# Kernel tuning notes

Measured on AMD Instinct MI355X. Metric: run time of the kernel, lower is better.

The kernel has to match this reference:

```python
import jax, jax.numpy as jnp
import numpy as np

B, T, D = 2, 2048, 1024
H, G, K = 16, 4, 64          # num_heads, num_kv_heads, head_dim
R = H // G                   # GQA repeat factor
F = 4096                     # mlp_dim
EPS = 1e-6


def rms_norm(x, scale, eps=EPS):
    var = jnp.mean(x.astype(jnp.float32) ** 2, axis=-1, keepdims=True)
    normed = x * jax.lax.rsqrt(var + eps)
    return (scale * normed).astype(x.dtype)


def apply_rope(x_BTHK, sin_BTK, cos_BTK):
    half = x_BTHK.shape[-1] // 2
    x1, x2 = x_BTHK[..., :half], x_BTHK[..., half:]
    s = sin_BTK[:, :, None, :]
    c = cos_BTK[:, :, None, :]
    return jnp.concatenate([x1 * c - x2 * s, x2 * c + x1 * s], axis=-1).astype(x_BTHK.dtype)


def setup_inputs() -> dict:
    key = jax.random.key(0)
    ks = jax.random.split(key, 12)
    hidden_BTD = jax.random.normal(ks[0], (B, T, D), jnp.float32)
    # rope tables: realistic sin/cos of position*inv_freq
    inv_freq = 1.0 / (10000.0 ** (jnp.arange(K // 2, dtype=jnp.float32) / (K // 2)))
    ang = jnp.arange(T, dtype=jnp.float32)[:, None] * inv_freq[None, :]  # [T, K/2]
    sin_BTK = jnp.broadcast_to(jnp.sin(ang)[None], (B, T, K // 2))
    cos_BTK = jnp.broadcast_to(jnp.cos(ang)[None], (B, T, K // 2))
    mask = jnp.broadcast_to(jnp.tril(jnp.ones((T, T), bool))[None], (B, T, T))
    sc = 1.0 / np.sqrt(D)
    scf = 1.0 / np.sqrt(F)
    return {
        "hidden_BTD": hidden_BTD, "sin_BTK": sin_BTK, "cos_BTK": cos_BTK, "mask": mask,
        "ln1_scale": jnp.ones((D,), jnp.float32),
        "ln2_scale": jnp.ones((D,), jnp.float32),
        "qn_scale": jnp.ones((K,), jnp.float32),
        "kn_scale": jnp.ones((K,), jnp.float32),
        "q_w": jax.random.normal(ks[1], (D, H * K), jnp.float32) * sc,
        "k_w": jax.random.normal(ks[2], (D, G * K), jnp.float32) * sc,
        "v_w": jax.random.normal(ks[3], (D, G * K), jnp.float32) * sc,
        "o_w": jax.random.normal(ks[4], (H * K, D), jnp.float32) * sc,
        "gate_w": jax.random.normal(ks[5], (D, F), jnp.float32) * sc,
        "up_w": jax.random.normal(ks[6], (D, F), jnp.float32) * sc,
        "down_w": jax.random.normal(ks[7], (F, D), jnp.float32) * scf,
    }


def reference(hidden_BTD, sin_BTK, cos_BTK, mask, ln1_scale, ln2_scale,
              qn_scale, kn_scale, q_w, k_w, v_w, o_w, gate_w, up_w, down_w):
    x = rms_norm(hidden_BTD, ln1_scale)
    q = rms_norm((x @ q_w).reshape(B, T, H, K), qn_scale)
    k = rms_norm((x @ k_w).reshape(B, T, G, K), kn_scale)
    v = (x @ v_w).reshape(B, T, G, K)
    q = apply_rope(q, sin_BTK, cos_BTK)
    k = apply_rope(k, sin_BTK, cos_BTK)
    q_BTGRK = q.reshape(B, T, G, R, K)
    scale = K ** (-0.5)
    logits = jnp.einsum('BTGRK,BSGK->BTSGR', q_BTGRK, k) * scale
    neg = float(jnp.finfo(logits.dtype).min)
    logits = jnp.where(mask[:, :, :, None, None], logits, neg)
    weights = jax.nn.softmax(logits.astype(jnp.float32), axis=2).astype(logits.dtype)
    attn = jnp.einsum('BTSGR,BSGK->BTGRK', weights, v).reshape(B, T, H * K)
    hidden_BTD = hidden_BTD + attn @ o_w
    y = rms_norm(hidden_BTD, ln2_scale)
    ff = (jax.nn.silu(y @ gate_w) * (y @ up_w)) @ down_w
    return hidden_BTD + ff
```

## Files before the change

kernel.cpp:

```cpp
#include <hip/hip_runtime.h>
#include <hip/hip_bf16.h>

#define EPSF 1e-6f
constexpr int Bsz  = 2;
constexpr int Tseq = 2048;
constexpr int Dmod = 1024;
constexpr int Hh   = 16;
constexpr int Gg   = 4;
constexpr int Ff   = 4096;
constexpr int Mrows = Bsz * Tseq;

typedef __attribute__((ext_vector_type(8))) short bf16x8;
typedef __attribute__((ext_vector_type(4))) float f32x4;
typedef unsigned short u16;

__device__ inline u16 f2bf(float x) {
    union { float f; unsigned u; } v; v.f = x;
    unsigned r = v.u + 0x7fff + ((v.u >> 16) & 1);
    return (u16)(r >> 16);
}
__device__ inline float bf2f(u16 h) {
    union { unsigned u; float f; } v; v.u = ((unsigned)h) << 16; return v.f;
}

__device__ __forceinline__ void async_copy16(const u16* g, u16* l) {
    __builtin_amdgcn_global_load_lds(
        (const __attribute__((address_space(1))) void*)g,
        (__attribute__((address_space(3))) void*)l, 16, 0, 0);
}


__global__ __launch_bounds__(256) void wprep_all_kernel(
    const float* __restrict__ q_w, const float* __restrict__ k_w,
    const float* __restrict__ v_w, const float* __restrict__ o_w,
    const float* __restrict__ gate_w, const float* __restrict__ up_w,
    const float* __restrict__ down_w,
    const float* __restrict__ hidden, const float* __restrict__ ln1,
    u16* __restrict__ QKVT, u16* __restrict__ OTh, u16* __restrict__ OTl,
    u16* __restrict__ GTh, u16* __restrict__ UTh, u16* __restrict__ DTh,
    u16* __restrict__ Xh)
{
    const int bx = blockIdx.x;

    if (bx >= 14848) {
        const int row = bx - 14848;
        const int tid = threadIdx.x;
        const float4 v = reinterpret_cast<const float4*>(hidden + (size_t)row * Dmod)[tid];
        float ss = v.x * v.x + v.y * v.y + v.z * v.z + v.w * v.w;
        #pragma unroll
        for (int off = 32; off; off >>= 1) ss += __shfl_xor(ss, off, 64);
        __shared__ float part[4];
        if ((tid & 63) == 0) part[tid >> 6] = ss;
        __syncthreads();
        const float tot = part[0] + part[1] + part[2] + part[3];
        const float rstd = rsqrtf(tot * (1.0f / Dmod) + EPSF);
        const float4 sc = reinterpret_cast<const float4*>(ln1)[tid];
        ushort4 h;
        h.x = f2bf(v.x * rstd * sc.x); h.y = f2bf(v.y * rstd * sc.y);
        h.z = f2bf(v.z * rstd * sc.z); h.w = f2bf(v.w * rstd * sc.w);
        *reinterpret_cast<ushort4*>(&Xh[(size_t)row * Dmod + tid * 4]) = h;
        return;
    }

    const float* W; u16* Th; u16* Tl = nullptr;
    int N, Kd, ntile, ktile, drow;
    if (bx < 1024) {
        W = q_w; N = 1024; Kd = 1024; ntile = bx & 31; ktile = bx >> 5;
        Th = QKVT; drow = ntile * 32;
    } else if (bx < 1280) {
        const int i = bx - 1024;
        W = k_w; N = 256; Kd = 1024; ntile = i & 7; ktile = i >> 3;
        Th = QKVT; drow = 1024 + ntile * 32;
    } else if (bx < 1536) {
        const int i = bx - 1280;
        W = v_w; N = 256; Kd = 1024; ntile = i & 7; ktile = i >> 3;
        Th = QKVT; drow = 1280 + ntile * 32;
    } else if (bx < 2560) {
        const int i = bx - 1536;
        W = o_w; N = 1024; Kd = 1024; ntile = i & 31; ktile = i >> 5;
        Th = OTh; Tl = OTl; drow = ntile * 32;
    } else if (bx < 6656) {
        const int i = bx - 2560;
        W = gate_w; N = 4096; Kd = 1024; ntile = i & 127; ktile = i >> 7;
        Th = GTh; drow = ntile * 32;
    } else if (bx < 10752) {
        const int i = bx - 6656;
        W = up_w; N = 4096; Kd = 1024; ntile = i & 127; ktile = i >> 7;
        Th = UTh; drow = ntile * 32;
    } else {
        const int i = bx - 10752;
        W = down_w; N = 1024; Kd = 4096; ntile = i & 31; ktile = i >> 5;
        Th = DTh; drow = ntile * 32;
    }
    const int n0 = ntile * 32, k0 = ktile * 32;

    __shared__ float tile[32][33];
    const int r = threadIdx.x >> 3, c4 = (threadIdx.x & 7) * 4;
    const float4 v = *reinterpret_cast<const float4*>(&W[(size_t)(k0 + r) * N + n0 + c4]);
    tile[r][c4 + 0] = v.x; tile[r][c4 + 1] = v.y;
    tile[r][c4 + 2] = v.z; tile[r][c4 + 3] = v.w;
    __syncthreads();
    const int nl = threadIdx.x >> 3, kq = (threadIdx.x & 7) * 4;
    float x0 = tile[kq + 0][nl], x1 = tile[kq + 1][nl];
    float x2 = tile[kq + 2][nl], x3 = tile[kq + 3][nl];
    ushort4 h;
    h.x = f2bf(x0); h.y = f2bf(x1); h.z = f2bf(x2); h.w = f2bf(x3);
    *reinterpret_cast<ushort4*>(&Th[(size_t)(drow + nl) * Kd + k0 + kq]) = h;
    if (Tl) {
        ushort4 l;
        l.x = f2bf(x0 - bf2f(h.x)); l.y = f2bf(x1 - bf2f(h.y));
        l.z = f2bf(x2 - bf2f(h.z)); l.w = f2bf(x3 - bf2f(h.w));
        *reinterpret_cast<ushort4*>(&Tl[(size_t)(drow + nl) * Kd + k0 + kq]) = l;
    }
}

template <int LO>
__global__ __launch_bounds__(256) void rmsnorm_split_kernel(
    const float* __restrict__ x, const float* __restrict__ scale,
    u16* __restrict__ oh, u16* __restrict__ ol)
{
    const int row = blockIdx.x;
    const int tid = threadIdx.x;
    const float4 v = reinterpret_cast<const float4*>(x + (size_t)row * Dmod)[tid];
    float ss = v.x * v.x + v.y * v.y + v.z * v.z + v.w * v.w;
    #pragma unroll
    for (int off = 32; off; off >>= 1) ss += __shfl_xor(ss, off, 64);
    __shared__ float part[4];
    if ((tid & 63) == 0) part[tid >> 6] = ss;
    __syncthreads();
    const float tot = part[0] + part[1] + part[2] + part[3];
    const float rstd = rsqrtf(tot * (1.0f / Dmod) + EPSF);
    const float4 sc = reinterpret_cast<const float4*>(scale)[tid];
    float o0 = v.x * rstd * sc.x, o1 = v.y * rstd * sc.y;
    float o2 = v.z * rstd * sc.z, o3 = v.w * rstd * sc.w;
    ushort4 h;
    h.x = f2bf(o0); h.y = f2bf(o1); h.z = f2bf(o2); h.w = f2bf(o3);
    *reinterpret_cast<ushort4*>(&oh[(size_t)row * Dmod + tid * 4]) = h;
    if (LO) {
        ushort4 l;
        l.x = f2bf(o0 - bf2f(h.x)); l.y = f2bf(o1 - bf2f(h.y));
        l.z = f2bf(o2 - bf2f(h.z)); l.w = f2bf(o3 - bf2f(h.w));
        *reinterpret_cast<ushort4*>(&ol[(size_t)row * Dmod + tid * 4]) = l;
    }
}

template <int NKT, int BN, int ASPLIT, int BSPLIT, int RES>
__global__ __launch_bounds__(256, 2) void mfma_gemm_pipe(
    const u16* __restrict__ Ah, const u16* __restrict__ Al,
    const u16* __restrict__ Bh, const u16* __restrict__ Bl,
    const float* __restrict__ res, float* __restrict__ C,
    int M, int N)
{
    constexpr int Kd = NKT * 32;
    constexpr int NT = (BN / 2) / 16;
    constexpr int NI = 2 + 2 * ASPLIT + (BN / 64) + (BN / 64) * BSPLIT;
    static_assert((NKT - 2) % 3 == 0, "main loop unroll-3");

    __shared__ u16 AsH[3][128 * 32];
    __shared__ u16 BsH[3][BN * 32];
    __shared__ u16 AsL[ASPLIT ? 3 : 1][128 * 32];
    __shared__ u16 BsL[BSPLIT ? 3 : 1][BN * 32];

    const int tid = threadIdx.x;
    const int lane = tid & 63, wave = tid >> 6;
    const int wm = (wave >> 1) * 64, wn = (wave & 1) * (BN / 2);
    const int m0 = blockIdx.y * 128, n0 = blockIdx.x * BN;
    const int fm = lane & 15, quad = lane >> 4;
    const int fsw = (fm >> 1) & 3;
    const int fcol = (quad ^ fsw) * 8;

    f32x4 acc[4][NT];
    #pragma unroll
    for (int i = 0; i < 4; ++i)
        #pragma unroll
        for (int j = 0; j < NT; ++j) acc[i][j] = (f32x4){0.f, 0.f, 0.f, 0.f};

    const int srow = tid >> 2;
    const int schk = tid & 3;
    const int sw   = schk ^ ((srow >> 1) & 3);
    const u16* aS0 = &Ah[(size_t)(m0 + srow) * Kd + sw * 8];
    const u16* aS1 = &Ah[(size_t)(m0 + srow + 64) * Kd + sw * 8];
    const u16* bS0 = &Bh[(size_t)(n0 + srow) * Kd + sw * 8];
    const u16* bS1 = (BN == 128) ? &Bh[(size_t)(n0 + srow + 64) * Kd + sw * 8] : nullptr;
    const u16* alS0 = ASPLIT ? &Al[(size_t)(m0 + srow) * Kd + sw * 8] : nullptr;
    const u16* alS1 = ASPLIT ? &Al[(size_t)(m0 + srow + 64) * Kd + sw * 8] : nullptr;
    const u16* blS0 = BSPLIT ? &Bl[(size_t)(n0 + srow) * Kd + sw * 8] : nullptr;
    const u16* blS1 = (BSPLIT && BN == 128) ? &Bl[(size_t)(n0 + srow + 64) * Kd + sw * 8] : nullptr;
    const int dst0 = srow * 32 + schk * 8;
    const int dst1 = dst0 + 64 * 32;

#define PSTAGE(T, BUF) do {                                                  \
        async_copy16(aS0 + (T) * 32, &AsH[BUF][dst0]);                       \
        async_copy16(aS1 + (T) * 32, &AsH[BUF][dst1]);                       \
        if (ASPLIT) {                                                        \
            async_copy16(alS0 + (T) * 32, &AsL[BUF][dst0]);                  \
            async_copy16(alS1 + (T) * 32, &AsL[BUF][dst1]);                  \
        }                                                                    \
        async_copy16(bS0 + (T) * 32, &BsH[BUF][dst0]);                       \
        if (BN == 128) async_copy16(bS1 + (T) * 32, &BsH[BUF][dst1]);        \
        if (BSPLIT) {                                                        \
            async_copy16(blS0 + (T) * 32, &BsL[BUF][dst0]);                  \
            if (BN == 128) async_copy16(blS1 + (T) * 32, &BsL[BUF][dst1]);   \
        }                                                                    \
    } while (0)

#define PGATE(GATE) do {                                                     \
        if ((GATE) == 1) {                                                   \
            if constexpr (NI == 3)                                           \
                asm volatile("s_waitcnt vmcnt(3)" ::: "memory");             \
            else if constexpr (NI == 4)                                      \
                asm volatile("s_waitcnt vmcnt(4)" ::: "memory");             \
            else if constexpr (NI == 6)                                      \
                asm volatile("s_waitcnt vmcnt(6)" ::: "memory");             \
            else                                                             \
                asm volatile("s_waitcnt vmcnt(8)" ::: "memory");             \
        } else if ((GATE) == 0) {                                            \
            asm volatile("s_waitcnt vmcnt(0)" ::: "memory");                 \
        }                                                                    \
    } while (0)

#define PSTEP(BC, BN_, T, PF, GATE) do {                                     \
    bf16x8 ah[4], bh[NT], al[4], bl[NT];                                     \
    _Pragma("unroll")                                                        \
    for (int t = 0; t < 4; ++t) {                                            \
        const int ra = (wm + t * 16 + fm) * 32 + fcol;                       \
        ah[t] = *reinterpret_cast<const bf16x8*>(&AsH[BC][ra]);              \
        if (ASPLIT) al[t] = *reinterpret_cast<const bf16x8*>(&AsL[BC][ra]);  \
    }                                                                        \
    _Pragma("unroll")                                                        \
    for (int t = 0; t < NT; ++t) {                                           \
        const int rb = (wn + t * 16 + fm) * 32 + fcol;                       \
        bh[t] = *reinterpret_cast<const bf16x8*>(&BsH[BC][rb]);              \
        if (BSPLIT) bl[t] = *reinterpret_cast<const bf16x8*>(&BsL[BC][rb]);  \
    }                                                                        \
    if (PF) PSTAGE((T) + 2, BN_);                                            \
    __builtin_amdgcn_s_setprio(1);                                           \
    _Pragma("unroll")                                                        \
    for (int mt = 0; mt < 4; ++mt)                                           \
        _Pragma("unroll")                                                    \
        for (int nt = 0; nt < NT; ++nt) {                                    \
            acc[mt][nt] = __builtin_amdgcn_mfma_f32_16x16x32_bf16(           \
                ah[mt], bh[nt], acc[mt][nt], 0, 0, 0);                       \
            if (BSPLIT)                                                      \
                acc[mt][nt] = __builtin_amdgcn_mfma_f32_16x16x32_bf16(       \
                    ah[mt], bl[nt], acc[mt][nt], 0, 0, 0);                   \
            if (ASPLIT)                                                      \
                acc[mt][nt] = __builtin_amdgcn_mfma_f32_16x16x32_bf16(       \
                    al[mt], bh[nt], acc[mt][nt], 0, 0, 0);                   \
        }                                                                    \
    __builtin_amdgcn_s_setprio(0);                                           \
    PGATE(GATE);                                                             \
    __builtin_amdgcn_s_barrier();                                            \
} while (0)

    PSTAGE(0, 0);
    PSTAGE(1, 1);
    PGATE(1);
    __builtin_amdgcn_s_barrier();

    #pragma unroll 1
    for (int t3 = 0; t3 < NKT - 2; t3 += 3) {
        PSTEP(0, 2, t3 + 0, true, 1);
        PSTEP(1, 0, t3 + 1, true, 1);
        PSTEP(2, 1, t3 + 2, true, 1);
    }
    PSTEP(0, 2, NKT - 2, false, 0);
    PSTEP(1, 0, NKT - 1, false, -1);

#undef PSTEP
#undef PGATE
#undef PSTAGE

    const int cr = (lane >> 4) * 4, cn = lane & 15;
    #pragma unroll
    for (int mt = 0; mt < 4; ++mt)
        #pragma unroll
        for (int nt = 0; nt < NT; ++nt)
            #pragma unroll
            for (int r = 0; r < 4; ++r) {
                const int gm = m0 + wm + mt * 16 + cr + r;
                const int gn = n0 + wn + nt * 16 + cn;
                float v = acc[mt][nt][r];
                if (RES) v += res[(size_t)gm * N + gn];
                C[(size_t)gm * N + gn] = v;
            }
}

__global__ __launch_bounds__(256, 2) void qkv_fused_kernel(
    const u16* __restrict__ Ah, const u16* __restrict__ Bh,
    const float* __restrict__ qn, const float* __restrict__ kn,
    const float* __restrict__ sinp, const float* __restrict__ cosp,
    u16* __restrict__ Qbh, u16* __restrict__ Qbl,
    u16* __restrict__ Kbh, u16* __restrict__ Kbl,
    u16* __restrict__ Vth, u16* __restrict__ Vtl)
{
    constexpr int Kd = 1024;
    constexpr int NKT = 32;
    __shared__ u16 As[3][128 * 32];
    __shared__ u16 Bs[3][128 * 32];

    const int tid = threadIdx.x;
    const int lane = tid & 63, wave = tid >> 6;
    const int wm = (wave >> 1) * 64, wn = (wave & 1) * 64;
    const int m0 = blockIdx.y * 128, n0 = blockIdx.x * 128;
    const int fm = lane & 15, quad = lane >> 4;
    const int fsw = (fm >> 1) & 3;
    const int fcol = ((quad ^ fsw) * 8);

    f32x4 acc[4][4];
    #pragma unroll
    for (int i = 0; i < 4; ++i)
        #pragma unroll
        for (int j = 0; j < 4; ++j) acc[i][j] = (f32x4){0.f, 0.f, 0.f, 0.f};

    const int srow = tid >> 2;
    const int schk = tid & 3;
    const int sw   = schk ^ ((srow >> 1) & 3);
    const u16* aS0 = &Ah[(size_t)(m0 + srow) * Kd + sw * 8];
    const u16* aS1 = &Ah[(size_t)(m0 + srow + 64) * Kd + sw * 8];
    const u16* bS0 = &Bh[(size_t)(n0 + srow) * Kd + sw * 8];
    const u16* bS1 = &Bh[(size_t)(n0 + srow + 64) * Kd + sw * 8];
    const int dst0 = srow * 32 + schk * 8;
    const int dst1 = dst0 + 64 * 32;

#define QSTAGE(T, BUF) do {                                                  \
        async_copy16(aS0 + (T) * 32, &As[BUF][dst0]);                        \
        async_copy16(aS1 + (T) * 32, &As[BUF][dst1]);                        \
        async_copy16(bS0 + (T) * 32, &Bs[BUF][dst0]);                        \
        async_copy16(bS1 + (T) * 32, &Bs[BUF][dst1]);                        \
    } while (0)

#define QSTEP(BC, BN, T, PF, GATE) do {                                      \
    bf16x8 ah[4], bh[4];                                                     \
    _Pragma("unroll")                                                        \
    for (int t = 0; t < 4; ++t) {                                            \
        ah[t] = *reinterpret_cast<const bf16x8*>(                            \
            &As[BC][(wm + t * 16 + fm) * 32 + fcol]);                        \
        bh[t] = *reinterpret_cast<const bf16x8*>(                            \
            &Bs[BC][(wn + t * 16 + fm) * 32 + fcol]);                        \
    }                                                                        \
    if (PF) QSTAGE((T) + 2, BN);                                             \
    __builtin_amdgcn_s_setprio(1);                                           \
    _Pragma("unroll")                                                        \
    for (int mt = 0; mt < 4; ++mt)                                           \
        _Pragma("unroll")                                                    \
        for (int nt = 0; nt < 4; ++nt)                                       \
            acc[mt][nt] = __builtin_amdgcn_mfma_f32_16x16x32_bf16(           \
                ah[mt], bh[nt], acc[mt][nt], 0, 0, 0);                       \
    __builtin_amdgcn_s_setprio(0);                                           \
    if ((GATE) == 1) {                                                       \
        asm volatile("s_waitcnt vmcnt(4)" ::: "memory");                     \
    } else if ((GATE) == 0) {                                                \
        asm volatile("s_waitcnt vmcnt(0)" ::: "memory");                     \
    }                                                                        \
    __builtin_amdgcn_s_barrier();                                            \
} while (0)

    QSTAGE(0, 0);
    QSTAGE(1, 1);
    asm volatile("s_waitcnt vmcnt(4)" ::: "memory");
    __builtin_amdgcn_s_barrier();

    #pragma unroll 1
    for (int t3 = 0; t3 < NKT - 2; t3 += 3) {
        QSTEP(0, 2, t3 + 0, true, 1);
        QSTEP(1, 0, t3 + 1, true, 1);
        QSTEP(2, 1, t3 + 2, true, 1);
    }
    QSTEP(0, 2, NKT - 2, false, 0);
    QSTEP(1, 0, NKT - 1, false, -1);

#undef QSTEP
#undef QSTAGE

    const int gn0 = n0 + wn;
    const int l15 = lane & 15;

    if (gn0 < 1280) {
        const bool isQ = (gn0 < 1024);
        const float* nsc = isQ ? qn : kn;
        const float osc = isQ ? 0.125f : 1.0f;
        u16* __restrict__ oh = isQ ? Qbh : Kbh;
        u16* __restrict__ ol = isQ ? Qbl : Kbl;
        const int rowstride = isQ ? 1024 : 256;
        const int colbase = isQ ? gn0 : gn0 - 1024;
        float sc[4];
        #pragma unroll
        for (int nt = 0; nt < 4; ++nt) sc[nt] = nsc[nt * 16 + l15];

        #pragma unroll
        for (int mt = 0; mt < 4; ++mt)
            #pragma unroll
            for (int r = 0; r < 4; ++r) {
                const int bt = m0 + wm + mt * 16 + quad * 4 + r;
                float v[4];
                #pragma unroll
                for (int nt = 0; nt < 4; ++nt) v[nt] = acc[mt][nt][r];
                float ss = v[0] * v[0] + v[1] * v[1] + v[2] * v[2] + v[3] * v[3];
                #pragma unroll
                for (int off = 1; off < 16; off <<= 1)
                    ss += __shfl_xor(ss, off, 16);
                const float rstd = rsqrtf(ss * (1.0f / 64.0f) + EPSF);
                float nv[4];
                #pragma unroll
                for (int nt = 0; nt < 4; ++nt) nv[nt] = v[nt] * rstd * sc[nt];
                const float s0 = sinp[bt * 32 + l15];
                const float c0 = cosp[bt * 32 + l15];
                const float s1 = sinp[bt * 32 + 16 + l15];
                const float c1 = cosp[bt * 32 + 16 + l15];
                float o[4];
                o[0] = (nv[0] * c0 - nv[2] * s0) * osc;
                o[1] = (nv[1] * c1 - nv[3] * s1) * osc;
                o[2] = (nv[2] * c0 + nv[0] * s0) * osc;
                o[3] = (nv[3] * c1 + nv[1] * s1) * osc;
                #pragma unroll
                for (int nt = 0; nt < 4; ++nt) {
                    const size_t off = (size_t)bt * rowstride + colbase + nt * 16 + l15;
                    const u16 hi = f2bf(o[nt]);
                    oh[off] = hi;
                    ol[off] = f2bf(o[nt] - bf2f(hi));
                }
            }
    } else {
        const int g = (gn0 - 1280) >> 6;
        const int b = (m0 + wm) >> 11;
        const int tb = ((m0 + wm) & 2047) + quad * 4;
        #pragma unroll
        for (int mt = 0; mt < 4; ++mt)
            #pragma unroll
            for (int nt = 0; nt < 4; ++nt) {
                const float v0 = acc[mt][nt][0], v1 = acc[mt][nt][1];
                const float v2 = acc[mt][nt][2], v3 = acc[mt][nt][3];
                ushort4 hv, lv;
                hv.x = f2bf(v0); hv.y = f2bf(v1); hv.z = f2bf(v2); hv.w = f2bf(v3);
                lv.x = f2bf(v0 - bf2f(hv.x)); lv.y = f2bf(v1 - bf2f(hv.y));
                lv.z = f2bf(v2 - bf2f(hv.z)); lv.w = f2bf(v3 - bf2f(hv.w));
                const size_t off =
                    ((size_t)((b * 4 + g) * 64 + nt * 16 + l15)) * Tseq + tb + mt * 16;
                *reinterpret_cast<ushort4*>(&Vth[off]) = hv;
                *reinterpret_cast<ushort4*>(&Vtl[off]) = lv;
            }
    }
}

#define GU_MFMA4(MBASE, AF)                                                      \
    _Pragma("unroll")                                                            \
    for (int mf = 0; mf < 4; ++mf) {                                             \
        accg[(MBASE) + mf][0] = __builtin_amdgcn_mfma_f32_16x16x32_bf16(         \
            AF[mf], bgf[0], accg[(MBASE) + mf][0], 0, 0, 0);                     \
        accu[(MBASE) + mf][0] = __builtin_amdgcn_mfma_f32_16x16x32_bf16(         \
            AF[mf], buf2[0], accu[(MBASE) + mf][0], 0, 0, 0);                    \
        accg[(MBASE) + mf][1] = __builtin_amdgcn_mfma_f32_16x16x32_bf16(         \
            AF[mf], bgf[1], accg[(MBASE) + mf][1], 0, 0, 0);                     \
        accu[(MBASE) + mf][1] = __builtin_amdgcn_mfma_f32_16x16x32_bf16(         \
            AF[mf], buf2[1], accu[(MBASE) + mf][1], 0, 0, 0);                    \
    }

__global__ __launch_bounds__(512, 2) void gateup8_kernel(
    const u16* __restrict__ Yh, const u16* __restrict__ Yl,
    const u16* __restrict__ Gw, const u16* __restrict__ Uw,
    u16* __restrict__ FF)
{
    constexpr int NK = 32;
    __shared__ u16 AsH[3][256 * 32];
    __shared__ u16 AsL[3][256 * 32];
    __shared__ u16 Gs[3][128 * 32];
    __shared__ u16 Us[3][128 * 32];

    const int tid  = threadIdx.x;
    const int lane = tid & 63;
    const int wave = tid >> 6;
    const int wave_m = wave >> 2;
    const int wave_n = wave & 3;

    const int wg  = blockIdx.x;
    const int xcd = wg & 7;
    const int idx = wg >> 3;
    const int ntile = xcd * 4 + (idx & 3);
    const int mtile = idx >> 2;
    const int m0 = mtile * 256, n0 = ntile * 128;

    const int fm = lane & 15, quad = lane >> 4;
    const int fsw = (fm >> 1) & 3;
    const int fcol = (quad ^ fsw) * 8;

    f32x4 accg[8][2], accu[8][2];
    #pragma unroll
    for (int i = 0; i < 8; ++i)
        #pragma unroll
        for (int j = 0; j < 2; ++j) {
            accg[i][j] = (f32x4){0.f, 0.f, 0.f, 0.f};
            accu[i][j] = (f32x4){0.f, 0.f, 0.f, 0.f};
        }

    const int srow = tid >> 2;
    const int schk = tid & 3;
    const int sw   = schk ^ ((srow >> 1) & 3);
    const u16* aSrc0 = &Yh[(size_t)(m0 + srow) * 1024 + sw * 8];
    const u16* aSrc1 = &Yh[(size_t)(m0 + srow + 128) * 1024 + sw * 8];
    const u16* lSrc0 = &Yl[(size_t)(m0 + srow) * 1024 + sw * 8];
    const u16* lSrc1 = &Yl[(size_t)(m0 + srow + 128) * 1024 + sw * 8];
    const u16* gSrc  = &Gw[(size_t)(n0 + srow) * 1024 + sw * 8];
    const u16* uSrc  = &Uw[(size_t)(n0 + srow) * 1024 + sw * 8];
    const int aDst0 = srow * 32 + schk * 8;
    const int aDst1 = aDst0 + 128 * 32;

#define STAGE_AH(T, BUF) do {                                  \
        async_copy16(aSrc0 + (T) * 32, &AsH[BUF][aDst0]);      \
        async_copy16(aSrc1 + (T) * 32, &AsH[BUF][aDst1]); } while (0)
#define STAGE_AL(T, BUF) do {                                  \
        async_copy16(lSrc0 + (T) * 32, &AsL[BUF][aDst0]);      \
        async_copy16(lSrc1 + (T) * 32, &AsL[BUF][aDst1]); } while (0)
#define STAGE_B(T, BUF) do {                                   \
        async_copy16(gSrc + (T) * 32, &Gs[BUF][aDst0]);        \
        async_copy16(uSrc + (T) * 32, &Us[BUF][aDst0]); } while (0)

    int raOff[8], rbOff[2];
    #pragma unroll
    for (int mf = 0; mf < 8; ++mf)
        raOff[mf] = (wave_m * 128 + mf * 16 + fm) * 32 + fcol;
    #pragma unroll
    for (int nf = 0; nf < 2; ++nf)
        rbOff[nf] = (wave_n * 32 + nf * 16 + fm) * 32 + fcol;

    STAGE_AH(0, 0); STAGE_AL(0, 0); STAGE_B(0, 0);
    STAGE_AH(1, 1); STAGE_AL(1, 1); STAGE_B(1, 1);
    asm volatile("s_waitcnt vmcnt(6)" ::: "memory");
    __builtin_amdgcn_s_barrier();

#define GU_STEP(BC, BN_, T, PF, GATE) do {                                   \
    bf16x8 bgf[2], buf2[2];                                                  \
    _Pragma("unroll")                                                        \
    for (int nf = 0; nf < 2; ++nf) {                                         \
        bgf[nf]  = *reinterpret_cast<const bf16x8*>(&Gs[BC][rbOff[nf]]);     \
        buf2[nf] = *reinterpret_cast<const bf16x8*>(&Us[BC][rbOff[nf]]);     \
    }                                                                        \
    {                                                                        \
        bf16x8 af[4];                                                        \
        _Pragma("unroll")                                                    \
        for (int mf = 0; mf < 4; ++mf)                                       \
            af[mf] = *reinterpret_cast<const bf16x8*>(&AsH[BC][raOff[mf]]);  \
        if (PF) STAGE_AH((T) + 2, BN_);                                      \
        __builtin_amdgcn_s_setprio(1);                                       \
        GU_MFMA4(0, af);                                                     \
        __builtin_amdgcn_s_setprio(0);                                       \
    }                                                                        \
    {                                                                        \
        bf16x8 af[4];                                                        \
        _Pragma("unroll")                                                    \
        for (int mf = 0; mf < 4; ++mf)                                       \
            af[mf] = *reinterpret_cast<const bf16x8*>(&AsH[BC][raOff[mf + 4]]); \
        if (PF) STAGE_AL((T) + 2, BN_);                                      \
        __builtin_amdgcn_s_setprio(1);                                       \
        GU_MFMA4(4, af);                                                     \
        __builtin_amdgcn_s_setprio(0);                                       \
    }                                                                        \
    {                                                                        \
        bf16x8 af[4];                                                        \
        _Pragma("unroll")                                                    \
        for (int mf = 0; mf < 4; ++mf)                                       \
            af[mf] = *reinterpret_cast<const bf16x8*>(&AsL[BC][raOff[mf]]);  \
        if (PF) STAGE_B((T) + 2, BN_);                                       \
        __builtin_amdgcn_s_setprio(1);                                       \
        GU_MFMA4(0, af);                                                     \
        __builtin_amdgcn_s_setprio(0);                                       \
    }                                                                        \
    {                                                                        \
        bf16x8 af[4];                                                        \
        _Pragma("unroll")                                                    \
        for (int mf = 0; mf < 4; ++mf)                                       \
            af[mf] = *reinterpret_cast<const bf16x8*>(&AsL[BC][raOff[mf + 4]]); \
        __builtin_amdgcn_s_setprio(1);                                       \
        GU_MFMA4(4, af);                                                     \
        __builtin_amdgcn_s_setprio(0);                                       \
    }                                                                        \
    if ((GATE) == 1) {                                                       \
        asm volatile("s_waitcnt vmcnt(6)" ::: "memory");                     \
    } else if ((GATE) == 0) {                                                \
        asm volatile("s_waitcnt vmcnt(0)" ::: "memory");                     \
    }                                                                        \
    __builtin_amdgcn_s_barrier();                                            \
} while (0)

    #pragma unroll 1
    for (int t3 = 0; t3 < NK - 2; t3 += 3) {
        GU_STEP(0, 2, t3 + 0, true, 1);
        GU_STEP(1, 0, t3 + 1, true, 1);
        GU_STEP(2, 1, t3 + 2, true, 1);
    }
    GU_STEP(0, 2, 30, false, 0);
    GU_STEP(1, 0, 31, false, -1);

#undef GU_STEP
#undef STAGE_AH
#undef STAGE_AL
#undef STAGE_B

    const int cr = quad * 4;
    #pragma unroll
    for (int mf = 0; mf < 8; ++mf)
        #pragma unroll
        for (int nf = 0; nf < 2; ++nf)
            #pragma unroll
            for (int r = 0; r < 4; ++r) {
                const int gm = m0 + wave_m * 128 + mf * 16 + cr + r;
                const int gn = n0 + wave_n * 32 + nf * 16 + fm;
                const float g = accg[mf][nf][r];
                const float ff = (g / (1.0f + __expf(-g))) * accu[mf][nf][r];
                FF[(size_t)gm * Ff + gn] = f2bf(ff);
            }
}

__global__ __launch_bounds__(512) void attn_mfma_kernel(
    const u16* __restrict__ Qh, const u16* __restrict__ Ql,
    const u16* __restrict__ Kh, const u16* __restrict__ Kl,
    const u16* __restrict__ Vth, const u16* __restrict__ Vtl,
    u16* __restrict__ AOh, u16* __restrict__ AOl)
{
    __shared__ u16 KsH[64 * 72];
    __shared__ u16 KsL[64 * 72];
    __shared__ u16 VsH[64 * 72];
    __shared__ u16 VsL[64 * 72];
    __shared__ u16 Ps[8][16 * 72];

    const int tid = threadIdx.x;
    const int wave = tid >> 6, lane = tid & 63;
    const int l15 = lane & 15, quad = lane >> 4;

    const int bg = blockIdx.x & 7;
    const int b = bg >> 2, g = bg & 3;
    const int pair = 63 - (blockIdx.x >> 3);
    const int win = pair * 2 + (wave >> 2);
    const int t0 = win * 16;
    const int h = g * 4 + (wave & 3);

    bf16x8 qh[2], ql[2];
    {
        const size_t qrow = (size_t)(b * Tseq + t0 + l15) * 1024 + h * 64;
        #pragma unroll
        for (int ks = 0; ks < 2; ++ks) {
            qh[ks] = *reinterpret_cast<const bf16x8*>(&Qh[qrow + ks * 32 + quad * 8]);
            ql[ks] = *reinterpret_cast<const bf16x8*>(&Ql[qrow + ks * 32 + quad * 8]);
        }
    }

    const int srow = tid >> 3;
    const int scol = (tid & 7) * 8;
    const size_t kgb = (size_t)(b * Tseq) * 256 + g * 64 + scol;
    const size_t vgb = (size_t)(bg * 64 + srow) * Tseq + scol;

    const int nit = (pair * 32 + 16) / 64 + 1;

    uint4 ck0, cl0, cv0, cw0;
    {
        const size_t ka = kgb + (size_t)srow * 256;
        ck0 = *reinterpret_cast<const uint4*>(&Kh[ka]);
        cl0 = *reinterpret_cast<const uint4*>(&Kl[ka]);
        cv0 = *reinterpret_cast<const uint4*>(&Vth[vgb]);
        cw0 = *reinterpret_cast<const uint4*>(&Vtl[vgb]);
    }

    f32x4 oacc[4];
    #pragma unroll
    for (int nt = 0; nt < 4; ++nt) oacc[nt] = (f32x4){0.f, 0.f, 0.f, 0.f};
    float m_r[4], l_r[4];
    #pragma unroll
    for (int r = 0; r < 4; ++r) { m_r[r] = -1e30f; l_r[r] = 0.0f; }

    u16* psw = &Ps[wave][0];
    const int lb = srow * 72 + scol;

    for (int it = 0; it < nit; ++it) {
        const int s0 = it * 64;
        const bool diag = (it == nit - 1);

        __syncthreads();
        *reinterpret_cast<uint4*>(&KsH[lb]) = ck0;
        *reinterpret_cast<uint4*>(&KsL[lb]) = cl0;
        *reinterpret_cast<uint4*>(&VsH[lb]) = cv0;
        *reinterpret_cast<uint4*>(&VsL[lb]) = cw0;
        if (it + 1 < nit) {
            const size_t ka = kgb + (size_t)(s0 + 64 + srow) * 256;
            ck0 = *reinterpret_cast<const uint4*>(&Kh[ka]);
            cl0 = *reinterpret_cast<const uint4*>(&Kl[ka]);
            const size_t va = vgb + s0 + 64;
            cv0 = *reinterpret_cast<const uint4*>(&Vth[va]);
            cw0 = *reinterpret_cast<const uint4*>(&Vtl[va]);
        }
        __syncthreads();

        f32x4 sacc[4];
        #pragma unroll
        for (int nt = 0; nt < 4; ++nt) sacc[nt] = (f32x4){0.f, 0.f, 0.f, 0.f};

        #pragma unroll
        for (int ks = 0; ks < 2; ++ks) {
            bf16x8 kfh[4], kfl[4];
            #pragma unroll
            for (int nt = 0; nt < 4; ++nt) {
                const int a = (nt * 16 + l15) * 72 + ks * 32 + quad * 8;
                kfh[nt] = *reinterpret_cast<const bf16x8*>(&KsH[a]);
                kfl[nt] = *reinterpret_cast<const bf16x8*>(&KsL[a]);
            }
            #pragma unroll
            for (int nt = 0; nt < 4; ++nt) {
                sacc[nt] = __builtin_amdgcn_mfma_f32_16x16x32_bf16(qh[ks], kfh[nt], sacc[nt], 0, 0, 0);
                sacc[nt] = __builtin_amdgcn_mfma_f32_16x16x32_bf16(ql[ks], kfh[nt], sacc[nt], 0, 0, 0);
                sacc[nt] = __builtin_amdgcn_mfma_f32_16x16x32_bf16(qh[ks], kfl[nt], sacc[nt], 0, 0, 0);
            }
        }

        if (diag) {
            #pragma unroll
            for (int nt = 0; nt < 4; ++nt) {
                const int sg = s0 + nt * 16 + l15;
                #pragma unroll
                for (int r = 0; r < 4; ++r)
                    if (sg > t0 + quad * 4 + r) sacc[nt][r] = -1e30f;
            }
        }

        #pragma unroll
        for (int r = 0; r < 4; ++r) {
            float mx = fmaxf(fmaxf(sacc[0][r], sacc[1][r]),
                             fmaxf(sacc[2][r], sacc[3][r]));
            #pragma unroll
            for (int off = 1; off < 16; off <<= 1)
                mx = fmaxf(mx, __shfl_xor(mx, off, 16));
            const float mnew = fmaxf(m_r[r], mx);
            const float alpha = __expf(m_r[r] - mnew);
            m_r[r] = mnew;

            float rs = 0.0f;
            #pragma unroll
            for (int nt = 0; nt < 4; ++nt) {
                const float p = __expf(sacc[nt][r] - mnew);
                sacc[nt][r] = p;
                rs += p;
            }
            #pragma unroll
            for (int off = 1; off < 16; off <<= 1)
                rs += __shfl_xor(rs, off, 16);
            l_r[r] = l_r[r] * alpha + rs;
            #pragma unroll
            for (int nt = 0; nt < 4; ++nt) oacc[nt][r] *= alpha;
            #pragma unroll
            for (int nt = 0; nt < 4; ++nt)
                psw[(quad * 4 + r) * 72 + nt * 16 + l15] = f2bf(sacc[nt][r]);
        }

        #pragma unroll
        for (int ks = 0; ks < 2; ++ks) {
            const bf16x8 pa = *reinterpret_cast<const bf16x8*>(
                &psw[l15 * 72 + ks * 32 + quad * 8]);
            bf16x8 vfh[4], vfl[4];
            #pragma unroll
            for (int nt = 0; nt < 4; ++nt) {
                const int a = (nt * 16 + l15) * 72 + ks * 32 + quad * 8;
                vfh[nt] = *reinterpret_cast<const bf16x8*>(&VsH[a]);
                vfl[nt] = *reinterpret_cast<const bf16x8*>(&VsL[a]);
            }
            #pragma unroll
            for (int nt = 0; nt < 4; ++nt) {
                oacc[nt] = __builtin_amdgcn_mfma_f32_16x16x32_bf16(pa, vfh[nt], oacc[nt], 0, 0, 0);
                oacc[nt] = __builtin_amdgcn_mfma_f32_16x16x32_bf16(pa, vfl[nt], oacc[nt], 0, 0, 0);
            }
        }
    }

    #pragma unroll
    for (int r = 0; r < 4; ++r) {
        const float inv = 1.0f / l_r[r];
        const size_t orow = (size_t)(b * Tseq + t0 + quad * 4 + r) * 1024 + h * 64;
        #pragma unroll
        for (int nt = 0; nt < 4; ++nt) {
            const float o = oacc[nt][r] * inv;
            const u16 hi = f2bf(o);
            AOh[orow + nt * 16 + l15] = hi;
            AOl[orow + nt * 16 + l15] = f2bf(o - bf2f(hi));
        }
    }
}

extern "C" void kernel_launch(void* const* d_in, const int* in_sizes, int n_in,
                              void* d_out, int out_size, void* d_ws,
                              size_t ws_size, hipStream_t stream)
{
    const float* hidden = (const float*)d_in[0];
    const float* sinp   = (const float*)d_in[1];
    const float* cosp   = (const float*)d_in[2];
    const float* ln1    = (const float*)d_in[4];
    const float* ln2    = (const float*)d_in[5];
    const float* qn     = (const float*)d_in[6];
    const float* kn     = (const float*)d_in[7];
    const float* q_w    = (const float*)d_in[8];
    const float* k_w    = (const float*)d_in[9];
    const float* v_w    = (const float*)d_in[10];
    const float* o_w    = (const float*)d_in[11];
    const float* gate_w = (const float*)d_in[12];
    const float* up_w   = (const float*)d_in[13];
    const float* down_w = (const float*)d_in[14];
    float* out = (float*)d_out;

    char* base = (char*)d_ws;
    u16*   OTh  = (u16*)(base);
    u16*   OTl  = (u16*)(base + 2097152);
    u16*   GTh  = (u16*)(base + 4194304);
    u16*   UTh  = (u16*)(base + 12582912);
    u16*   DTh  = (u16*)(base + 20971520);
    u16*   QKVT = (u16*)(base + 29360128);
    u16*   Xh   = (u16*)(base + 32505856);
    u16*   Qbh  = (u16*)(base + 40894464);
    u16*   Qbl  = (u16*)(base + 49283072);
    u16*   Kbh  = (u16*)(base + 57671680);
    u16*   Kbl  = (u16*)(base + 59768832);
    u16*   Vth  = (u16*)(base + 61865984);
    u16*   Vtl  = (u16*)(base + 63963136);
    u16*   AOh  = (u16*)(base + 66060288);
    u16*   AOl  = (u16*)(base + 74448896);
    u16*   FFh  = (u16*)(base + 82837504);

    float* H2 = (float*)Qbh;
    u16*   Yh = Kbh;
    u16*   Yl = AOh;

    wprep_all_kernel<<<14848 + Mrows, 256, 0, stream>>>(
        q_w, k_w, v_w, o_w, gate_w, up_w, down_w, hidden, ln1,
        QKVT, OTh, OTl, GTh, UTh, DTh, Xh);

    qkv_fused_kernel<<<dim3(12, 32), 256, 0, stream>>>(
        Xh, QKVT, qn, kn, sinp, cosp, Qbh, Qbl, Kbh, Kbl, Vth, Vtl);

    attn_mfma_kernel<<<Bsz * Gg * (Tseq / 32), 512, 0, stream>>>(
        Qbh, Qbl, Kbh, Kbl, Vth, Vtl, AOh, AOl);

    mfma_gemm_pipe<32, 128, 1, 1, 1><<<dim3(8, 32), 256, 0, stream>>>(
        AOh, AOl, OTh, OTl, hidden, H2, Mrows, Dmod);

    rmsnorm_split_kernel<1><<<Mrows, 256, 0, stream>>>(H2, ln2, Yh, Yl);

    gateup8_kernel<<<512, 512, 0, stream>>>(Yh, Yl, GTh, UTh, FFh);

    mfma_gemm_pipe<128, 128, 0, 0, 1><<<dim3(8, 32), 256, 0, stream>>>(
        FFh, nullptr, DTh, nullptr, H2, out, Mrows, Dmod);
}
```

Before: 475.6 us.

## Deepen GEMM shared-memory pipeline from 3 to 4 buffers with prefetch distance 3

Both MFMA GEMM kernels now rotate through four LDS buffers instead of three and prefetch the tile three steps ahead instead of two. The vmcnt waits are adjusted to allow two stages in flight, and the prologue and epilogue are rewritten for a 4-way unrolled loop. The goal is to hide more global-load latency behind MFMA work. In exchange each block uses a third more LDS, which may reduce occupancy below the two blocks per CU requested in the launch bounds.

```diff
diff --git a/kernel.cpp b/kernel.cpp
--- a/kernel.cpp
+++ b/kernel.cpp
@@ -154,12 +154,12 @@
     constexpr int Kd = NKT * 32;
     constexpr int NT = (BN / 2) / 16;
     constexpr int NI = 2 + 2 * ASPLIT + (BN / 64) + (BN / 64) * BSPLIT;
-    static_assert((NKT - 2) % 3 == 0, "main loop unroll-3");
-
-    __shared__ u16 AsH[3][128 * 32];
-    __shared__ u16 BsH[3][BN * 32];
-    __shared__ u16 AsL[ASPLIT ? 3 : 1][128 * 32];
-    __shared__ u16 BsL[BSPLIT ? 3 : 1][BN * 32];
+    static_assert(NKT % 4 == 0 && NKT >= 8, "4-buffer rotation");
+
+    __shared__ u16 AsH[4][128 * 32];
+    __shared__ u16 BsH[4][BN * 32];
+    __shared__ u16 AsL[ASPLIT ? 4 : 1][128 * 32];
+    __shared__ u16 BsL[BSPLIT ? 4 : 1][BN * 32];
 
     const int tid = threadIdx.x;
     const int lane = tid & 63, wave = tid >> 6;
@@ -205,13 +205,14 @@
     } while (0)
 
 #define PGATE(GATE) do {                                                     \
-        if ((GATE) == 1) {                                                   \
-            if constexpr (NI == 3)                                           \
-                asm volatile("s_waitcnt vmcnt(3)" ::: "memory");             \
-            else if constexpr (NI == 4)                                      \
+        if ((GATE) == 2) {                                                   \
+            if constexpr (NI == 4)                                           \
+                asm volatile("s_waitcnt vmcnt(8)" ::: "memory");             \
+            else                                                             \
+                asm volatile("s_waitcnt vmcnt(16)" ::: "memory");            \
+        } else if ((GATE) == 1) {                                            \
+            if constexpr (NI == 4)                                           \
                 asm volatile("s_waitcnt vmcnt(4)" ::: "memory");             \
-            else if constexpr (NI == 6)                                      \
-                asm volatile("s_waitcnt vmcnt(6)" ::: "memory");             \
             else                                                             \
                 asm volatile("s_waitcnt vmcnt(8)" ::: "memory");             \
         } else if ((GATE) == 0) {                                            \
@@ -233,7 +234,7 @@
         bh[t] = *reinterpret_cast<const bf16x8*>(&BsH[BC][rb]);              \
         if (BSPLIT) bl[t] = *reinterpret_cast<const bf16x8*>(&BsL[BC][rb]);  \
     }                                                                        \
-    if (PF) PSTAGE((T) + 2, BN_);                                            \
+    if (PF) PSTAGE((T) + 3, BN_);                                            \
     __builtin_amdgcn_s_setprio(1);                                           \
     _Pragma("unroll")                                                        \
     for (int mt = 0; mt < 4; ++mt)                                           \
@@ -255,17 +256,21 @@
 
     PSTAGE(0, 0);
     PSTAGE(1, 1);
-    PGATE(1);
+    PSTAGE(2, 2);
+    PGATE(2);
     __builtin_amdgcn_s_barrier();
 
     #pragma unroll 1
-    for (int t3 = 0; t3 < NKT - 2; t3 += 3) {
-        PSTEP(0, 2, t3 + 0, true, 1);
-        PSTEP(1, 0, t3 + 1, true, 1);
-        PSTEP(2, 1, t3 + 2, true, 1);
-    }
-    PSTEP(0, 2, NKT - 2, false, 0);
-    PSTEP(1, 0, NKT - 1, false, -1);
+    for (int t4 = 0; t4 < NKT - 4; t4 += 4) {
+        PSTEP((t4 + 0) & 3, (t4 + 3) & 3, t4 + 0, true, 2);
+        PSTEP((t4 + 1) & 3, (t4 + 0) & 3, t4 + 1, true, 2);
+        PSTEP((t4 + 2) & 3, (t4 + 1) & 3, t4 + 2, true, 2);
+        PSTEP((t4 + 3) & 3, (t4 + 2) & 3, t4 + 3, true, 2);
+    }
+    PSTEP(0, 3, NKT - 4, true, 2);
+    PSTEP(1, 0, NKT - 3, false, 1);
+    PSTEP(2, 1, NKT - 2, false, 0);
+    PSTEP(3, 2, NKT - 1, false, -1);
 
 #undef PSTEP
 #undef PGATE
@@ -296,8 +301,8 @@
 {
     constexpr int Kd = 1024;
     constexpr int NKT = 32;
-    __shared__ u16 As[3][128 * 32];
-    __shared__ u16 Bs[3][128 * 32];
+    __shared__ u16 As[4][128 * 32];
+    __shared__ u16 Bs[4][128 * 32];
 
     const int tid = threadIdx.x;
     const int lane = tid & 63, wave = tid >> 6;
@@ -339,7 +344,7 @@
         bh[t] = *reinterpret_cast<const bf16x8*>(                            \
             &Bs[BC][(wn + t * 16 + fm) * 32 + fcol]);                        \
     }                                                                        \
-    if (PF) QSTAGE((T) + 2, BN);                                             \
+    if (PF) QSTAGE((T) + 3, BN);                                             \
     __builtin_amdgcn_s_setprio(1);                                           \
     _Pragma("unroll")                                                        \
     for (int mt = 0; mt < 4; ++mt)                                           \
@@ -348,7 +353,9 @@
             acc[mt][nt] = __builtin_amdgcn_mfma_f32_16x16x32_bf16(           \
                 ah[mt], bh[nt], acc[mt][nt], 0, 0, 0);                       \
     __builtin_amdgcn_s_setprio(0);                                           \
-    if ((GATE) == 1) {                                                       \
+    if ((GATE) == 2) {                                                       \
+        asm volatile("s_waitcnt vmcnt(8)" ::: "memory");                     \
+    } else if ((GATE) == 1) {                                                \
         asm volatile("s_waitcnt vmcnt(4)" ::: "memory");                     \
     } else if ((GATE) == 0) {                                                \
         asm volatile("s_waitcnt vmcnt(0)" ::: "memory");                     \
@@ -358,17 +365,21 @@
 
     QSTAGE(0, 0);
     QSTAGE(1, 1);
-    asm volatile("s_waitcnt vmcnt(4)" ::: "memory");
+    QSTAGE(2, 2);
+    asm volatile("s_waitcnt vmcnt(8)" ::: "memory");
     __builtin_amdgcn_s_barrier();
 
     #pragma unroll 1
-    for (int t3 = 0; t3 < NKT - 2; t3 += 3) {
-        QSTEP(0, 2, t3 + 0, true, 1);
-        QSTEP(1, 0, t3 + 1, true, 1);
-        QSTEP(2, 1, t3 + 2, true, 1);
-    }
-    QSTEP(0, 2, NKT - 2, false, 0);
-    QSTEP(1, 0, NKT - 1, false, -1);
+    for (int t4 = 0; t4 < NKT - 4; t4 += 4) {
+        QSTEP((t4 + 0) & 3, (t4 + 3) & 3, t4 + 0, true, 2);
+        QSTEP((t4 + 1) & 3, (t4 + 0) & 3, t4 + 1, true, 2);
+        QSTEP((t4 + 2) & 3, (t4 + 1) & 3, t4 + 2, true, 2);
+        QSTEP((t4 + 3) & 3, (t4 + 2) & 3, t4 + 3, true, 2);
+    }
+    QSTEP(0, 3, NKT - 4, true, 2);
+    QSTEP(1, 0, NKT - 3, false, 1);
+    QSTEP(2, 1, NKT - 2, false, 0);
+    QSTEP(3, 2, NKT - 1, false, -1);
 
 #undef QSTEP
 #undef QSTAGE
```

Result: slower. 490.0 us (+3.0%).
